# Optimization experiments

Hardware: AMD Instinct MI355X
Metric: run time of the kernel (lower is better)

The kernel has to match this reference:

```python
import jax, jax.numpy as jnp
import numpy as np

B, T = 4096, 16384

def setup_inputs() -> dict:
    key = jax.random.key(0)
    ks = jax.random.split(key, 6)
    x = jax.random.normal(ks[0], (B, T), dtype=jnp.float32)
    v0 = jnp.zeros((B, 2), dtype=jnp.float32)
    # match torch init ranges: b* ~ U(-1,1), a* ~ U(-0.5,0.5) (stable region)
    b0 = jax.random.uniform(ks[1], (1,), jnp.float32, -1.0, 1.0)
    b1 = jax.random.uniform(ks[2], (1,), jnp.float32, -1.0, 1.0)
    b2 = jax.random.uniform(ks[3], (1,), jnp.float32, -1.0, 1.0)
    a1 = jax.random.uniform(ks[4], (1,), jnp.float32, -0.5, 0.5)
    a2 = jax.random.uniform(ks[5], (1,), jnp.float32, -0.5, 0.5)
    return {"x": x, "v0": v0, "b0": b0, "b1": b1, "b2": b2, "a1": a1, "a2": a2}

def reference(x, v0, b0, b1, b2, a1, a2):
    """DF-II transposed biquad, scanned over time.
    x: [B, T] input samples; v0: [B, 2] initial state.
    Returns (y [B, T], v_final [B, 2]).
    Per-step math is exactly DTDFIICell.forward:
      y   = x_t * b0 + v[:,0]
      v0' = x_t * b1 + v[:,1] - y * a1
      v1' = x_t * b2            - y * a2
    """
    def step(v, xt):  # v: [B,2], xt: [B]
        y = xt * b0 + v[:, 0]                      # [B]
        v_new = jnp.stack(
            [xt * b1 + v[:, 1] - y * a1,
             xt * b2 - y * a2], axis=-1)           # [B,2]
        return v_new, y
    v_final, ys = jax.lax.scan(step, v0, x.T)      # ys: [T, B]
    return ys.T, v_final
```

## Files before the change

### kernel.cpp

```cpp
#include <hip/hip_runtime.h>

#define B_DIM 4096
#define T_DIM 16384
#define WAVES_PER_BLOCK 4
#define CHUNK 256

struct M2 { float a, b, c, d; };

__device__ inline M2 m2mul(const M2& X, const M2& Y) {
    M2 r;
    r.a = fmaf(X.a, Y.a, X.b * Y.c);
    r.b = fmaf(X.a, Y.b, X.b * Y.d);
    r.c = fmaf(X.c, Y.a, X.d * Y.c);
    r.d = fmaf(X.c, Y.b, X.d * Y.d);
    return r;
}

__global__ __launch_bounds__(256) void biquad_scan_kernel(
    const float* __restrict__ x, const float* __restrict__ v0in,
    const float* __restrict__ pb0, const float* __restrict__ pb1,
    const float* __restrict__ pb2, const float* __restrict__ pa1,
    const float* __restrict__ pa2,
    float* __restrict__ y, float* __restrict__ vout)
{
    const int lane = threadIdx.x & 63;
    const int wave = threadIdx.x >> 6;
    const int row  = blockIdx.x * WAVES_PER_BLOCK + wave;
    if (row >= B_DIM) return;

    const float b0 = *pb0, b1 = *pb1, b2 = *pb2, a1 = *pa1, a2 = *pa2;
    const float c0 = b1 - a1 * b0;
    const float c1 = b2 - a2 * b0;

    M2 A  { -a1, 1.0f, -a2, 0.0f };
    M2 A2 = m2mul(A, A);
    M2 A4 = m2mul(A2, A2);

    M2 S0, S1, S2, S3, S4, S5;
    M2 Q { 1.f, 0.f, 0.f, 1.f };
    M2 M = A4;
    S0 = M; if (lane & 1)  Q = m2mul(M, Q); M = m2mul(M, M);
    S1 = M; if (lane & 2)  Q = m2mul(M, Q); M = m2mul(M, M);
    S2 = M; if (lane & 4)  Q = m2mul(M, Q); M = m2mul(M, M);
    S3 = M; if (lane & 8)  Q = m2mul(M, Q); M = m2mul(M, M);
    S4 = M; if (lane & 16) Q = m2mul(M, Q); M = m2mul(M, M);
    S5 = M; if (lane & 32) Q = m2mul(M, Q); M = m2mul(M, M);
    const M2 R = M;

    const float*  xr = x + (size_t)row * T_DIM;
    float*        yr = y + (size_t)row * T_DIM;

    float vc0 = v0in[row * 2 + 0];
    float vc1 = v0in[row * 2 + 1];

    const int NIT = T_DIM / CHUNK;

    float4 xv = ((const float4*)(xr))[lane];
    float4 xn = ((const float4*)(xr + CHUNK))[lane];

    for (int i = 0; i < NIT; ++i) {
        float4 xn2 = make_float4(0.f, 0.f, 0.f, 0.f);
        if (i + 2 < NIT) xn2 = ((const float4*)(xr + (size_t)(i + 2) * CHUNK))[lane];

        float d0 = c0 * xv.x;
        float d1 = c1 * xv.x;
        {   float t0 = fmaf(c0, xv.y, fmaf(-a1, d0, d1));
            float t1 = fmaf(-a2, d0, c1 * xv.y);
            d0 = t0; d1 = t1; }
        {   float t0 = fmaf(c0, xv.z, fmaf(-a1, d0, d1));
            float t1 = fmaf(-a2, d0, c1 * xv.z);
            d0 = t0; d1 = t1; }
        {   float t0 = fmaf(c0, xv.w, fmaf(-a1, d0, d1));
            float t1 = fmaf(-a2, d0, c1 * xv.w);
            d0 = t0; d1 = t1; }

        #define SCAN_STEP(Sm, o)                                        \
        {   float p0 = __shfl_up(d0, (unsigned)(o));                    \
            float p1 = __shfl_up(d1, (unsigned)(o));                    \
            if (lane < (o)) { p0 = 0.f; p1 = 0.f; }                     \
            float t0 = fmaf(Sm.a, p0, fmaf(Sm.b, p1, d0));              \
            float t1 = fmaf(Sm.c, p0, fmaf(Sm.d, p1, d1));              \
            d0 = t0; d1 = t1; }
        SCAN_STEP(S0, 1)
        SCAN_STEP(S1, 2)
        SCAN_STEP(S2, 4)
        SCAN_STEP(S3, 8)
        SCAN_STEP(S4, 16)
        SCAN_STEP(S5, 32)
        #undef SCAN_STEP

        float e0 = __shfl_up(d0, 1u);
        float e1 = __shfl_up(d1, 1u);
        if (lane == 0) { e0 = 0.f; e1 = 0.f; }

        float v0r = fmaf(Q.a, vc0, fmaf(Q.b, vc1, e0));
        float v1r = fmaf(Q.c, vc0, fmaf(Q.d, vc1, e1));

        float4 yv;
        {   float xs = xv.x; float yy = fmaf(xs, b0, v0r);
            float n0 = fmaf(-a1, yy, fmaf(xs, b1, v1r));
            float n1 = fmaf(-a2, yy, xs * b2);
            v0r = n0; v1r = n1; yv.x = yy; }
        {   float xs = xv.y; float yy = fmaf(xs, b0, v0r);
            float n0 = fmaf(-a1, yy, fmaf(xs, b1, v1r));
            float n1 = fmaf(-a2, yy, xs * b2);
            v0r = n0; v1r = n1; yv.y = yy; }
        {   float xs = xv.z; float yy = fmaf(xs, b0, v0r);
            float n0 = fmaf(-a1, yy, fmaf(xs, b1, v1r));
            float n1 = fmaf(-a2, yy, xs * b2);
            v0r = n0; v1r = n1; yv.z = yy; }
        {   float xs = xv.w; float yy = fmaf(xs, b0, v0r);
            float n0 = fmaf(-a1, yy, fmaf(xs, b1, v1r));
            float n1 = fmaf(-a2, yy, xs * b2);
            v0r = n0; v1r = n1; yv.w = yy; }

        ((float4*)(yr + (size_t)i * CHUNK))[lane] = yv;

        float t0 = __shfl(d0, 63);
        float t1 = __shfl(d1, 63);
        float nv0 = fmaf(R.a, vc0, fmaf(R.b, vc1, t0));
        float nv1 = fmaf(R.c, vc0, fmaf(R.d, vc1, t1));
        vc0 = nv0; vc1 = nv1;

        xv = xn; xn = xn2;
    }

    if (lane == 0) {
        vout[row * 2 + 0] = vc0;
        vout[row * 2 + 1] = vc1;
    }
}

extern "C" void kernel_launch(void* const* d_in, const int* in_sizes, int n_in,
                              void* d_out, int out_size, void* d_ws, size_t ws_size,
                              hipStream_t stream) {
    const float* x   = (const float*)d_in[0];
    const float* v0  = (const float*)d_in[1];
    const float* b0  = (const float*)d_in[2];
    const float* b1  = (const float*)d_in[3];
    const float* b2  = (const float*)d_in[4];
    const float* a1  = (const float*)d_in[5];
    const float* a2  = (const float*)d_in[6];

    float* y    = (float*)d_out;
    float* vout = (float*)d_out + (size_t)B_DIM * T_DIM;

    dim3 grid(B_DIM / WAVES_PER_BLOCK);
    dim3 block(64 * WAVES_PER_BLOCK);
    biquad_scan_kernel<<<grid, block, 0, stream>>>(x, v0, b0, b1, b2, a1, a2, y, vout);
}
```

Baseline: 109.2 us.

## Process 8 samples per lane and compute outputs in parallel from the zero-state pass

Each lane now handles 8 consecutive samples instead of 4, which halves the number of wave-level shuffle scan iterations. The serial output recurrence is replaced by a closed form: the zero-state pass records partial outputs, and each output is corrected with precomputed powers of the state matrix applied to the incoming state. This takes the second sequential dependency chain off the critical path. The change also adds nontemporal loads and stores, and sets launch bounds to 4 for occupancy, at the cost of more registers.

```diff
diff --git a/kernel.cpp b/kernel.cpp
--- a/kernel.cpp
+++ b/kernel.cpp
@@ -3,7 +3,10 @@
 #define B_DIM 4096
 #define T_DIM 16384
 #define WAVES_PER_BLOCK 4
-#define CHUNK 256
+#define PER_LANE 8
+#define CHUNK (64 * PER_LANE)
+
+typedef float f32x4 __attribute__((ext_vector_type(4)));
 
 struct M2 { float a, b, c, d; };
 
@@ -16,7 +19,7 @@
     return r;
 }
 
-__global__ __launch_bounds__(256) void biquad_scan_kernel(
+__global__ __launch_bounds__(256, 4) void biquad_scan_kernel(
     const float* __restrict__ x, const float* __restrict__ v0in,
     const float* __restrict__ pb0, const float* __restrict__ pb1,
     const float* __restrict__ pb2, const float* __restrict__ pa1,
@@ -29,16 +32,30 @@
     if (row >= B_DIM) return;
 
     const float b0 = *pb0, b1 = *pb1, b2 = *pb2, a1 = *pa1, a2 = *pa2;
+    const float na1 = -a1, na2 = -a2;
     const float c0 = b1 - a1 * b0;
     const float c1 = b2 - a2 * b0;
 
-    M2 A  { -a1, 1.0f, -a2, 0.0f };
+    M2 A  { na1, 1.0f, na2, 0.0f };
     M2 A2 = m2mul(A, A);
+    M2 A3 = m2mul(A2, A);
     M2 A4 = m2mul(A2, A2);
+    M2 A5 = m2mul(A4, A);
+    M2 A6 = m2mul(A4, A2);
+    M2 A7 = m2mul(A4, A3);
+    M2 A8 = m2mul(A4, A4);
+
+    const float p1a = A .a, p1b = A .b;
+    const float p2a = A2.a, p2b = A2.b;
+    const float p3a = A3.a, p3b = A3.b;
+    const float p4a = A4.a, p4b = A4.b;
+    const float p5a = A5.a, p5b = A5.b;
+    const float p6a = A6.a, p6b = A6.b;
+    const float p7a = A7.a, p7b = A7.b;
 
     M2 S0, S1, S2, S3, S4, S5;
     M2 Q { 1.f, 0.f, 0.f, 1.f };
-    M2 M = A4;
+    M2 M = A8;
     S0 = M; if (lane & 1)  Q = m2mul(M, Q); M = m2mul(M, M);
     S1 = M; if (lane & 2)  Q = m2mul(M, Q); M = m2mul(M, M);
     S2 = M; if (lane & 4)  Q = m2mul(M, Q); M = m2mul(M, M);
@@ -47,39 +64,48 @@
     S5 = M; if (lane & 32) Q = m2mul(M, Q); M = m2mul(M, M);
     const M2 R = M;
 
-    const float*  xr = x + (size_t)row * T_DIM;
-    float*        yr = y + (size_t)row * T_DIM;
+    const float* xr = x + (size_t)row * T_DIM;
+    float*       yr = y + (size_t)row * T_DIM;
 
     float vc0 = v0in[row * 2 + 0];
     float vc1 = v0in[row * 2 + 1];
 
     const int NIT = T_DIM / CHUNK;
+    const int STEP4 = CHUNK / 4;
 
-    float4 xv = ((const float4*)(xr))[lane];
-    float4 xn = ((const float4*)(xr + CHUNK))[lane];
+    const f32x4* xp = (const f32x4*)xr + lane * 2;
+    f32x4*       yp = (f32x4*)yr + lane * 2;
+
+    f32x4 ca = __builtin_nontemporal_load(&xp[0]);
+    f32x4 cb = __builtin_nontemporal_load(&xp[1]);
+    xp += STEP4;
+    f32x4 pa = __builtin_nontemporal_load(&xp[0]);
+    f32x4 pb = __builtin_nontemporal_load(&xp[1]);
 
     for (int i = 0; i < NIT; ++i) {
-        float4 xn2 = make_float4(0.f, 0.f, 0.f, 0.f);
-        if (i + 2 < NIT) xn2 = ((const float4*)(xr + (size_t)(i + 2) * CHUNK))[lane];
+        f32x4 ma = {0.f, 0.f, 0.f, 0.f}, mb = {0.f, 0.f, 0.f, 0.f};
+        if (i + 2 < NIT) {
+            ma = __builtin_nontemporal_load(&xp[STEP4]);
+            mb = __builtin_nontemporal_load(&xp[STEP4 + 1]);
+        }
 
-        float d0 = c0 * xv.x;
-        float d1 = c1 * xv.x;
-        {   float t0 = fmaf(c0, xv.y, fmaf(-a1, d0, d1));
-            float t1 = fmaf(-a2, d0, c1 * xv.y);
+        float d0 = 0.f, d1 = 0.f;
+        float yz0, yz1, yz2, yz3, yz4, yz5, yz6, yz7;
+        #define FOLD(xs, yz)                                           \
+        {   yz = fmaf((xs), b0, d0);                                   \
+            float t0 = fmaf(c0, (xs), fmaf(na1, d0, d1));              \
+            float t1 = fmaf(na2, d0, c1 * (xs));                       \
             d0 = t0; d1 = t1; }
-        {   float t0 = fmaf(c0, xv.z, fmaf(-a1, d0, d1));
-            float t1 = fmaf(-a2, d0, c1 * xv.z);
-            d0 = t0; d1 = t1; }
-        {   float t0 = fmaf(c0, xv.w, fmaf(-a1, d0, d1));
-            float t1 = fmaf(-a2, d0, c1 * xv.w);
-            d0 = t0; d1 = t1; }
+        FOLD(ca[0], yz0) FOLD(ca[1], yz1) FOLD(ca[2], yz2) FOLD(ca[3], yz3)
+        FOLD(cb[0], yz4) FOLD(cb[1], yz5) FOLD(cb[2], yz6) FOLD(cb[3], yz7)
+        #undef FOLD
 
         #define SCAN_STEP(Sm, o)                                        \
-        {   float p0 = __shfl_up(d0, (unsigned)(o));                    \
-            float p1 = __shfl_up(d1, (unsigned)(o));                    \
-            if (lane < (o)) { p0 = 0.f; p1 = 0.f; }                     \
-            float t0 = fmaf(Sm.a, p0, fmaf(Sm.b, p1, d0));              \
-            float t1 = fmaf(Sm.c, p0, fmaf(Sm.d, p1, d1));              \
+        {   float q0 = __shfl_up(d0, (unsigned)(o));                    \
+            float q1 = __shfl_up(d1, (unsigned)(o));                    \
+            if (lane < (o)) { q0 = 0.f; q1 = 0.f; }                     \
+            float t0 = fmaf(Sm.a, q0, fmaf(Sm.b, q1, d0));              \
+            float t1 = fmaf(Sm.c, q0, fmaf(Sm.d, q1, d1));              \
             d0 = t0; d1 = t1; }
         SCAN_STEP(S0, 1)
         SCAN_STEP(S1, 2)
@@ -93,28 +119,21 @@
         float e1 = __shfl_up(d1, 1u);
         if (lane == 0) { e0 = 0.f; e1 = 0.f; }
 
-        float v0r = fmaf(Q.a, vc0, fmaf(Q.b, vc1, e0));
-        float v1r = fmaf(Q.c, vc0, fmaf(Q.d, vc1, e1));
+        const float vb0 = fmaf(Q.a, vc0, fmaf(Q.b, vc1, e0));
+        const float vb1 = fmaf(Q.c, vc0, fmaf(Q.d, vc1, e1));
 
-        float4 yv;
-        {   float xs = xv.x; float yy = fmaf(xs, b0, v0r);
-            float n0 = fmaf(-a1, yy, fmaf(xs, b1, v1r));
-            float n1 = fmaf(-a2, yy, xs * b2);
-            v0r = n0; v1r = n1; yv.x = yy; }
-        {   float xs = xv.y; float yy = fmaf(xs, b0, v0r);
-            float n0 = fmaf(-a1, yy, fmaf(xs, b1, v1r));
-            float n1 = fmaf(-a2, yy, xs * b2);
-            v0r = n0; v1r = n1; yv.y = yy; }
-        {   float xs = xv.z; float yy = fmaf(xs, b0, v0r);
-            float n0 = fmaf(-a1, yy, fmaf(xs, b1, v1r));
-            float n1 = fmaf(-a2, yy, xs * b2);
-            v0r = n0; v1r = n1; yv.z = yy; }
-        {   float xs = xv.w; float yy = fmaf(xs, b0, v0r);
-            float n0 = fmaf(-a1, yy, fmaf(xs, b1, v1r));
-            float n1 = fmaf(-a2, yy, xs * b2);
-            v0r = n0; v1r = n1; yv.w = yy; }
+        f32x4 yo0, yo1;
+        yo0[0] = yz0 + vb0;
+        yo0[1] = fmaf(p1a, vb0, fmaf(p1b, vb1, yz1));
+        yo0[2] = fmaf(p2a, vb0, fmaf(p2b, vb1, yz2));
+        yo0[3] = fmaf(p3a, vb0, fmaf(p3b, vb1, yz3));
+        yo1[0] = fmaf(p4a, vb0, fmaf(p4b, vb1, yz4));
+        yo1[1] = fmaf(p5a, vb0, fmaf(p5b, vb1, yz5));
+        yo1[2] = fmaf(p6a, vb0, fmaf(p6b, vb1, yz6));
+        yo1[3] = fmaf(p7a, vb0, fmaf(p7b, vb1, yz7));
 
-        ((float4*)(yr + (size_t)i * CHUNK))[lane] = yv;
+        __builtin_nontemporal_store(yo0, &yp[0]);
+        __builtin_nontemporal_store(yo1, &yp[1]);
 
         float t0 = __shfl(d0, 63);
         float t1 = __shfl(d1, 63);
@@ -122,7 +141,9 @@
         float nv1 = fmaf(R.c, vc0, fmaf(R.d, vc1, t1));
         vc0 = nv0; vc1 = nv1;
 
-        xv = xn; xn = xn2;
+        ca = pa; cb = pb; pa = ma; pb = mb;
+        xp += STEP4;
+        yp += STEP4;
     }
 
     if (lane == 0) {
```

Result: slower. 124.9 us (+14.3%).
